# Kernel tuning notes

Hardware: AMD Instinct MI355X
Metric: run time of the kernel (lower is better)

Reference implementation:

```python
import jax, jax.numpy as jnp
import numpy as np

B_, K_, D_, L_, N_, R_ = 2, 4, 128, 4096, 16, 8


def setup_inputs() -> dict:
    key = jax.random.key(0)
    ks = jax.random.split(key, 7)
    return {
        "q_x": jax.random.normal(ks[0], (B_, K_, D_, L_), jnp.float32),
        "kv_x": jax.random.normal(ks[1], (B_, K_, D_, L_), jnp.float32),
        "x_proj_weight": jax.random.normal(ks[2], (K_, R_ + 2 * N_, D_), jnp.float32) * 0.02,
        "dt_projs_weight": jax.random.normal(ks[3], (K_, D_, R_), jnp.float32) * 0.02,
        "dt_projs_bias": jax.random.normal(ks[4], (K_, D_), jnp.float32) * 0.1,
        "A_logs": jax.random.uniform(ks[5], (K_ * D_, N_), jnp.float32),
        "Ds": jax.random.normal(ks[6], (K_ * D_,), jnp.float32),
    }


def _selective_scan(u, delta, A, Bmat, Cmat, Ds):
    # u, delta: [B,K,D,L]; A: [K,D,N]; Bmat, Cmat: [B,K,N,L]; Ds: [K,D]
    uT = jnp.moveaxis(u, -1, 0)      # [L,B,K,D]
    dT = jnp.moveaxis(delta, -1, 0)  # [L,B,K,D]
    BT = jnp.moveaxis(Bmat, -1, 0)   # [L,B,K,N]
    CT = jnpp if False else jnp.moveaxis(Cmat, -1, 0)  # [L,B,K,N]
    h0 = jnp.zeros(u.shape[:3] + (A.shape[-1],), jnp.float32)  # [B,K,D,N]

    def step(h, xs):
        u_l, d_l, B_l, C_l = xs
        dA = jnp.exp(d_l[..., None] * A)  # [B,K,D,N]
        h = dA * h + (d_l * u_l)[..., None] * B_l[:, :, None, :]
        y = jnp.einsum('bkdn,bkn->bkd', h, C_l)
        return h, y

    _, yT = jax.lax.scan(step, h0, (uT, dT, BT, CT))
    y = jnp.moveaxis(yT, 0, -1)  # [B,K,D,L]
    return y + u * Ds[None, :, :, None]


def reference(q_x, kv_x, x_proj_weight, dt_projs_weight, dt_projs_bias, A_logs, Ds):
    B, K, D, L = kv_x.shape
    N = A_logs.shape[1]
    R = dt_projs_weight.shape[2]
    # projections of kv (for dt, B) and q (for C)
    x_dbl = jnp.einsum('bkdl,kcd->bkcl', kv_x, x_proj_weight)
    x_c = jnp.einsum('bkdl,kcd->bkcl', q_x, x_proj_weight)
    dts = x_dbl[:, :, :R]          # [B,K,R,L]
    Bs = x_dbl[:, :, R:R + N]      # [B,K,N,L]
    Cs = x_c[:, :, R + N:]         # [B,K,N,L]
    dts = jnp.einsum('bkrl,kdr->bkdl', dts, dt_projs_weight)
    A = -jnp.exp(A_logs.astype(jnp.float32)).reshape(K, D, N)
    delta = jax.nn.softplus(dts.astype(jnp.float32) + dt_projs_bias.astype(jnp.float32)[None, :, :, None])
    y = _selective_scan(kv_x.astype(jnp.float32), delta, A,
                        Bs.astype(jnp.float32), Cs.astype(jnp.float32),
                        Ds.astype(jnp.float32).reshape(K, D))
    return y  # [B,K,D,L] float32
```

## Files before the change

### kernel.cpp

```cpp
#include <hip/hip_runtime.h>
#include <cmath>

namespace {
constexpr int B_ = 2, K_ = 4, D_ = 128, L_ = 4096, N_ = 16, R_ = 8, C_ = 40;
constexpr int CHUNK = 32, NCH = L_ / CHUNK;
constexpr float LOG2E = 1.44269504f;
}

#if __has_builtin(__builtin_amdgcn_exp2f)
#define FEXP2(x) __builtin_amdgcn_exp2f(x)
#else
#define FEXP2(x) exp2f(x)
#endif

__global__ __launch_bounds__(640, 2) void k1_proj(
    const float* __restrict__ qx, const float* __restrict__ kv,
    const float* __restrict__ xw,
    float* __restrict__ dtsT,
    float* __restrict__ BT,
    float* __restrict__ CT)
{
    __shared__ float Wt[D_ * C_];

    const int tid = threadIdx.x;
    const int w = tid >> 6, lane = tid & 63;
    const int dg = lane >> 5, lq = lane & 31;
    int blk = blockIdx.x;
    const int lt = blk & 31; blk >>= 5;
    const int k = blk & 3; const int b = blk >> 2;
    const int bk = b * K_ + k;

    for (int i = tid; i < C_ * D_; i += 640) {
        const int c = i >> 7, d = i & 127;
        Wt[d * C_ + c] = xw[(k * C_ + c) * D_ + d];
    }
    __syncthreads();

    const float* xsrc = (w >= 6) ? qx : kv;
    const int c0 = w * 4;
    float acc[4][4];
    #pragma unroll
    for (int c = 0; c < 4; ++c)
        #pragma unroll
        for (int j = 0; j < 4; ++j) acc[c][j] = 0.f;

    const float* src = xsrc + ((size_t)bk * D_ + dg * 64) * L_ + lt * 128 + 4 * lq;
    #pragma unroll 8
    for (int dd = 0; dd < 64; ++dd) {
        const float4 x = *(const float4*)(src + (size_t)dd * L_);
        const float4 wv = *(const float4*)&Wt[(dg * 64 + dd) * C_ + c0];
        const float* wp = (const float*)&wv;
        #pragma unroll
        for (int c = 0; c < 4; ++c) {
            acc[c][0] = fmaf(x.x, wp[c], acc[c][0]);
            acc[c][1] = fmaf(x.y, wp[c], acc[c][1]);
            acc[c][2] = fmaf(x.z, wp[c], acc[c][2]);
            acc[c][3] = fmaf(x.w, wp[c], acc[c][3]);
        }
    }

    #pragma unroll
    for (int c = 0; c < 4; ++c)
        #pragma unroll
        for (int j = 0; j < 4; ++j)
            acc[c][j] += __shfl_xor(acc[c][j], 32, 64);

    if (dg == 0) {
        #pragma unroll
        for (int j = 0; j < 4; ++j) {
            const int l = lt * 128 + 4 * lq + j;
            float4 o; o.x = acc[0][j]; o.y = acc[1][j]; o.z = acc[2][j]; o.w = acc[3][j];
            if (w < 2)
                *(float4*)(dtsT + ((size_t)bk * L_ + l) * R_ + w * 4) = o;
            else if (w < 6)
                *(float4*)(BT + ((size_t)bk * L_ + l) * N_ + (w - 2) * 4) = o;
            else
                *(float4*)(CT + ((size_t)bk * L_ + l) * N_ + (w - 6) * 4) = o;
        }
    }
}

__global__ __launch_bounds__(128, 1) void k2_pass1(
    const float* __restrict__ kv, const float* __restrict__ dtsT,
    const float* __restrict__ BT, const float* __restrict__ alg,
    const float* __restrict__ dtw, const float* __restrict__ dtb,
    float* __restrict__ hend, float* __restrict__ Ssum)
{
    __shared__ float dts_s[CHUNK * R_];
    __shared__ float B_s[CHUNK * N_];

    const int tid = threadIdx.x;
    const int d = tid;
    const int blk = blockIdx.x;
    const int ch = blk & (NCH - 1);
    const int bk = blk >> 7;
    const int k = bk & 3;

    {
        const float* src = dtsT + ((size_t)bk * L_ + ch * CHUNK) * R_;
        if (tid < 64) *(float4*)&dts_s[4 * tid] = *(const float4*)(src + 4 * tid);
        const float* bsrc = BT + ((size_t)bk * L_ + ch * CHUNK) * N_;
        *(float4*)&B_s[4 * tid] = *(const float4*)(bsrc + 4 * tid);
    }

    float uu[CHUNK];
    {
        const float4* up = (const float4*)(kv + ((size_t)bk * D_ + d) * L_ + ch * CHUNK);
        #pragma unroll
        for (int j = 0; j < 8; ++j) {
            const float4 v = up[j];
            uu[4*j] = v.x; uu[4*j+1] = v.y; uu[4*j+2] = v.z; uu[4*j+3] = v.w;
        }
    }

    float dtwr[R_];
    {
        const float* p = dtw + ((size_t)k * D_ + d) * R_;
        *(float4*)&dtwr[0] = *(const float4*)p;
        *(float4*)&dtwr[4] = *(const float4*)(p + 4);
    }
    const float bias = dtb[k * D_ + d];
    float A2[N_];
    {
        const float* ap = alg + ((size_t)k * D_ + d) * N_;
        #pragma unroll
        for (int j = 0; j < 4; ++j) {
            float4 a = *(const float4*)(ap + 4 * j);
            A2[4*j]   = -__expf(a.x) * LOG2E; A2[4*j+1] = -__expf(a.y) * LOG2E;
            A2[4*j+2] = -__expf(a.z) * LOG2E; A2[4*j+3] = -__expf(a.w) * LOG2E;
        }
    }
    __syncthreads();

    float h[N_];
    #pragma unroll
    for (int n = 0; n < N_; ++n) h[n] = 0.f;
    float sd = 0.f;

    #pragma unroll
    for (int l = 0; l < CHUNK; ++l) {
        float dv[R_];
        *(float4*)&dv[0] = *(const float4*)&dts_s[l * R_];
        *(float4*)&dv[4] = *(const float4*)&dts_s[l * R_ + 4];
        float s = bias;
        #pragma unroll
        for (int r = 0; r < R_; ++r) s = fmaf(dv[r], dtwr[r], s);
        const float e = FEXP2(s * LOG2E);
        const float dlt = (s > 15.f) ? s : __logf(1.f + e);
        sd += dlt;
        const float xb = dlt * uu[l];
        #pragma unroll
        for (int g = 0; g < 4; ++g) {
            const float4 bg = *(const float4*)&B_s[l * N_ + 4 * g];
            h[4*g+0] = fmaf(FEXP2(dlt * A2[4*g+0]), h[4*g+0], xb * bg.x);
            h[4*g+1] = fmaf(FEXP2(dlt * A2[4*g+1]), h[4*g+1], xb * bg.y);
            h[4*g+2] = fmaf(FEXP2(dlt * A2[4*g+2]), h[4*g+2], xb * bg.z);
            h[4*g+3] = fmaf(FEXP2(dlt * A2[4*g+3]), h[4*g+3], xb * bg.w);
        }
    }

    float* hp = hend + (((size_t)bk * NCH + ch) * D_ + d) * N_;
    #pragma unroll
    for (int j = 0; j < 4; ++j) {
        float4 o; o.x = h[4*j]; o.y = h[4*j+1]; o.z = h[4*j+2]; o.w = h[4*j+3];
        *(float4*)(hp + 4 * j) = o;
    }
    Ssum[((size_t)bk * NCH + ch) * D_ + d] = sd;
}

__global__ __launch_bounds__(64, 2) void k25_chain(
    const float* __restrict__ alg, const float* __restrict__ Ssum,
    const float* __restrict__ hend, float* __restrict__ hinit)
{
    const int tg = blockIdx.x * 64 + threadIdx.x;
    const int n = tg & 15;
    const int d = (tg >> 4) & 127;
    const int bk = tg >> 11;
    const int k = bk & 3;

    const float A2 = -__expf(alg[((size_t)k * D_ + d) * N_ + n]) * LOG2E;
    float h = 0.f;
    for (int c0 = 0; c0 < NCH; c0 += 32) {
        float he[32], ss[32];
        #pragma unroll
        for (int j = 0; j < 32; ++j) {
            const size_t si = ((size_t)bk * NCH + c0 + j) * D_ + d;
            he[j] = hend[si * N_ + n];
            ss[j] = Ssum[si];
        }
        #pragma unroll
        for (int j = 0; j < 32; ++j) {
            const size_t si = ((size_t)bk * NCH + c0 + j) * D_ + d;
            hinit[si * N_ + n] = h;
            h = fmaf(FEXP2(ss[j] * A2), h, he[j]);
        }
    }
}

__global__ __launch_bounds__(128, 1) void k3_pass2(
    const float* __restrict__ kv, const float* __restrict__ dtsT,
    const float* __restrict__ BT, const float* __restrict__ CT,
    const float* __restrict__ alg, const float* __restrict__ dtw,
    const float* __restrict__ dtb, const float* __restrict__ DsG,
    const float* __restrict__ hinit, float* __restrict__ out)
{
    constexpr int YS = CHUNK + 1;
    __shared__ float dts_s[CHUNK * R_];
    __shared__ float B_s[CHUNK * N_];
    __shared__ float C_s[CHUNK * N_];
    __shared__ float y_s[D_ * YS];

    const int tid = threadIdx.x;
    const int d = tid;
    const int blk = blockIdx.x;
    const int ch = blk & (NCH - 1);
    const int bk = blk >> 7;
    const int k = bk & 3;

    {
        const float* src = dtsT + ((size_t)bk * L_ + ch * CHUNK) * R_;
        if (tid < 64) *(float4*)&dts_s[4 * tid] = *(const float4*)(src + 4 * tid);
        const float* bsrc = BT + ((size_t)bk * L_ + ch * CHUNK) * N_;
        *(float4*)&B_s[4 * tid] = *(const float4*)(bsrc + 4 * tid);
        const float* csrc = CT + ((size_t)bk * L_ + ch * CHUNK) * N_;
        *(float4*)&C_s[4 * tid] = *(const float4*)(csrc + 4 * tid);
    }

    float uu[CHUNK];
    {
        const float4* up = (const float4*)(kv + ((size_t)bk * D_ + d) * L_ + ch * CHUNK);
        #pragma unroll
        for (int j = 0; j < 8; ++j) {
            const float4 v = up[j];
            uu[4*j] = v.x; uu[4*j+1] = v.y; uu[4*j+2] = v.z; uu[4*j+3] = v.w;
        }
    }

    float dtwr[R_];
    {
        const float* p = dtw + ((size_t)k * D_ + d) * R_;
        *(float4*)&dtwr[0] = *(const float4*)p;
        *(float4*)&dtwr[4] = *(const float4*)(p + 4);
    }
    const float bias = dtb[k * D_ + d];
    const float Dv = DsG[k * D_ + d];
    float A2[N_];
    {
        const float* ap = alg + ((size_t)k * D_ + d) * N_;
        #pragma unroll
        for (int j = 0; j < 4; ++j) {
            float4 a = *(const float4*)(ap + 4 * j);
            A2[4*j]   = -__expf(a.x) * LOG2E; A2[4*j+1] = -__expf(a.y) * LOG2E;
            A2[4*j+2] = -__expf(a.z) * LOG2E; A2[4*j+3] = -__expf(a.w) * LOG2E;
        }
    }

    float h[N_];
    {
        const float* hp = hinit + (((size_t)bk * NCH + ch) * D_ + d) * N_;
        #pragma unroll
        for (int j = 0; j < 4; ++j) {
            float4 v = *(const float4*)(hp + 4 * j);
            h[4*j] = v.x; h[4*j+1] = v.y; h[4*j+2] = v.z; h[4*j+3] = v.w;
        }
    }
    __syncthreads();

    #pragma unroll
    for (int l = 0; l < CHUNK; ++l) {
        float dv[R_];
        *(float4*)&dv[0] = *(const float4*)&dts_s[l * R_];
        *(float4*)&dv[4] = *(const float4*)&dts_s[l * R_ + 4];
        float s = bias;
        #pragma unroll
        for (int r = 0; r < R_; ++r) s = fmaf(dv[r], dtwr[r], s);
        const float e = FEXP2(s * LOG2E);
        const float dlt = (s > 15.f) ? s : __logf(1.f + e);
        const float xb = dlt * uu[l];
        float p0 = 0.f, p1 = 0.f;
        #pragma unroll
        for (int g = 0; g < 4; ++g) {
            const float4 bg = *(const float4*)&B_s[l * N_ + 4 * g];
            const float4 cg = *(const float4*)&C_s[l * N_ + 4 * g];
            h[4*g+0] = fmaf(FEXP2(dlt * A2[4*g+0]), h[4*g+0], xb * bg.x);
            p0 = fmaf(h[4*g+0], cg.x, p0);
            h[4*g+1] = fmaf(FEXP2(dlt * A2[4*g+1]), h[4*g+1], xb * bg.y);
            p1 = fmaf(h[4*g+1], cg.y, p1);
            h[4*g+2] = fmaf(FEXP2(dlt * A2[4*g+2]), h[4*g+2], xb * bg.z);
            p0 = fmaf(h[4*g+2], cg.z, p0);
            h[4*g+3] = fmaf(FEXP2(dlt * A2[4*g+3]), h[4*g+3], xb * bg.w);
            p1 = fmaf(h[4*g+3], cg.w, p1);
        }
        y_s[d * YS + l] = fmaf(uu[l], Dv, p0 + p1);
    }
    __syncthreads();

    #pragma unroll
    for (int p = 0; p < 8; ++p) {
        const int f = tid + p * 128;
        const int row = f >> 3, j4 = (f & 7) * 4;
        const float* yp = &y_s[row * YS + j4];
        float4 o; o.x = yp[0]; o.y = yp[1]; o.z = yp[2]; o.w = yp[3];
        *(float4*)(out + ((size_t)bk * D_ + row) * L_ + ch * CHUNK + j4) = o;
    }
}

extern "C" void kernel_launch(void* const* d_in, const int* in_sizes, int n_in,
                              void* d_out, int out_size, void* d_ws, size_t ws_size,
                              hipStream_t stream)
{
    const float* qx  = (const float*)d_in[0];
    const float* kv  = (const float*)d_in[1];
    const float* xw  = (const float*)d_in[2];
    const float* dtw = (const float*)d_in[3];
    const float* dtb = (const float*)d_in[4];
    const float* alg = (const float*)d_in[5];
    const float* Ds  = (const float*)d_in[6];
    float* out = (float*)d_out;

    const size_t sz_dts = (size_t)B_ * K_ * L_ * R_;
    const size_t sz_bc  = (size_t)B_ * K_ * L_ * N_;
    const size_t sz_h   = (size_t)B_ * K_ * NCH * D_ * N_;
    const size_t sz_ss  = (size_t)B_ * K_ * NCH * D_;
    const size_t need = (sz_dts + 2 * sz_bc + 2 * sz_h + sz_ss) * sizeof(float);
    if (ws_size < need) return;

    float* dts   = (float*)d_ws;
    float* BTp   = dts + sz_dts;
    float* CTp   = BTp + sz_bc;
    float* hend  = CTp + sz_bc;
    float* hinit = hend + sz_h;
    float* Ssm   = hinit + sz_h;

    k1_proj<<<B_ * K_ * 32, 640, 0, stream>>>(qx, kv, xw, dts, BTp, CTp);
    k2_pass1<<<B_ * K_ * NCH, 128, 0, stream>>>(kv, dts, BTp, alg, dtw, dtb, hend, Ssm);
    k25_chain<<<256, 64, 0, stream>>>(alg, Ssm, hend, hinit);
    k3_pass2<<<B_ * K_ * NCH, 128, 0, stream>>>(kv, dts, BTp, CTp, alg, dtw, dtb, Ds, hinit, out);
}
```

Baseline: 63.74 us.

## Fuse projection and scan pass-1 kernels into one launch

Merges the x-projection kernel and the first chunked-scan pass into one kernel of 512 threads per block. Each block computes the dt, B and C projections for 128 positions and writes them to the workspace. After a block barrier it reloads dt and B into shared memory and runs the pass-1 scan over four 32-long chunks. This removes one kernel launch and the inter-kernel gap. In exchange, the projection now has 8 waves for 10 jobs, so two waves do double work. It also relies on global writes being visible within the block after __syncthreads.

```diff
diff --git a/kernel.cpp b/kernel.cpp
--- a/kernel.cpp
+++ b/kernel.cpp
@@ -13,95 +13,86 @@
 #define FEXP2(x) exp2f(x)
 #endif
 
-__global__ __launch_bounds__(640, 2) void k1_proj(
+__global__ __launch_bounds__(512) void kA_proj_pass1(
     const float* __restrict__ qx, const float* __restrict__ kv,
-    const float* __restrict__ xw,
-    float* __restrict__ dtsT,
-    float* __restrict__ BT,
-    float* __restrict__ CT)
+    const float* __restrict__ xw, const float* __restrict__ dtw,
+    const float* __restrict__ dtb, const float* __restrict__ alg,
+    float* __restrict__ dtsT, float* __restrict__ BT, float* __restrict__ CT,
+    float* __restrict__ hend, float* __restrict__ Ssum)
 {
     __shared__ float Wt[D_ * C_];
+    __shared__ float dts_s[128 * R_];
+    __shared__ float B_s[128 * N_];
 
     const int tid = threadIdx.x;
     const int w = tid >> 6, lane = tid & 63;
-    const int dg = lane >> 5, lq = lane & 31;
-    int blk = blockIdx.x;
-    const int lt = blk & 31; blk >>= 5;
-    const int k = blk & 3; const int b = blk >> 2;
-    const int bk = b * K_ + k;
-
-    for (int i = tid; i < C_ * D_; i += 640) {
-        const int c = i >> 7, d = i & 127;
-        Wt[d * C_ + c] = xw[(k * C_ + c) * D_ + d];
-    }
-    __syncthreads();
-
-    const float* xsrc = (w >= 6) ? qx : kv;
-    const int c0 = w * 4;
-    float acc[4][4];
-    #pragma unroll
-    for (int c = 0; c < 4; ++c)
-        #pragma unroll
-        for (int j = 0; j < 4; ++j) acc[c][j] = 0.f;
-
-    const float* src = xsrc + ((size_t)bk * D_ + dg * 64) * L_ + lt * 128 + 4 * lq;
-    #pragma unroll 8
-    for (int dd = 0; dd < 64; ++dd) {
-        const float4 x = *(const float4*)(src + (size_t)dd * L_);
-        const float4 wv = *(const float4*)&Wt[(dg * 64 + dd) * C_ + c0];
-        const float* wp = (const float*)&wv;
-        #pragma unroll
-        for (int c = 0; c < 4; ++c) {
-            acc[c][0] = fmaf(x.x, wp[c], acc[c][0]);
-            acc[c][1] = fmaf(x.y, wp[c], acc[c][1]);
-            acc[c][2] = fmaf(x.z, wp[c], acc[c][2]);
-            acc[c][3] = fmaf(x.w, wp[c], acc[c][3]);
-        }
-    }
-
-    #pragma unroll
-    for (int c = 0; c < 4; ++c)
-        #pragma unroll
-        for (int j = 0; j < 4; ++j)
-            acc[c][j] += __shfl_xor(acc[c][j], 32, 64);
-
-    if (dg == 0) {
-        #pragma unroll
-        for (int j = 0; j < 4; ++j) {
-            const int l = lt * 128 + 4 * lq + j;
-            float4 o; o.x = acc[0][j]; o.y = acc[1][j]; o.z = acc[2][j]; o.w = acc[3][j];
-            if (w < 2)
-                *(float4*)(dtsT + ((size_t)bk * L_ + l) * R_ + w * 4) = o;
-            else if (w < 6)
-                *(float4*)(BT + ((size_t)bk * L_ + l) * N_ + (w - 2) * 4) = o;
-            else
-                *(float4*)(CT + ((size_t)bk * L_ + l) * N_ + (w - 6) * 4) = o;
-        }
-    }
-}
-
-__global__ __launch_bounds__(128, 1) void k2_pass1(
-    const float* __restrict__ kv, const float* __restrict__ dtsT,
-    const float* __restrict__ BT, const float* __restrict__ alg,
-    const float* __restrict__ dtw, const float* __restrict__ dtb,
-    float* __restrict__ hend, float* __restrict__ Ssum)
-{
-    __shared__ float dts_s[CHUNK * R_];
-    __shared__ float B_s[CHUNK * N_];
-
-    const int tid = threadIdx.x;
-    const int d = tid;
-    const int blk = blockIdx.x;
-    const int ch = blk & (NCH - 1);
-    const int bk = blk >> 7;
-    const int k = bk & 3;
-
-    {
-        const float* src = dtsT + ((size_t)bk * L_ + ch * CHUNK) * R_;
-        if (tid < 64) *(float4*)&dts_s[4 * tid] = *(const float4*)(src + 4 * tid);
-        const float* bsrc = BT + ((size_t)bk * L_ + ch * CHUNK) * N_;
-        *(float4*)&B_s[4 * tid] = *(const float4*)(bsrc + 4 * tid);
-    }
+    const int bk = blockIdx.x >> 5;
+    const int k  = bk & 3;
+    const int lt = blockIdx.x & 31;
+
+    for (int i = tid; i < C_ * D_; i += 512) {
+        const int c = i >> 7, dd = i & 127;
+        Wt[dd * C_ + c] = xw[(k * C_ + c) * D_ + dd];
+    }
+    __syncthreads();
+    {
+        const int dg = lane >> 5, lq = lane & 31;
+        for (int job = w; job < 10; job += 8) {
+            const float* xsrc = (job >= 6) ? qx : kv;
+            const int c0 = job * 4;
+            float acc[4][4];
+            #pragma unroll
+            for (int c = 0; c < 4; ++c)
+                #pragma unroll
+                for (int j = 0; j < 4; ++j) acc[c][j] = 0.f;
+
+            const float* src = xsrc + ((size_t)bk * D_ + dg * 64) * L_ + lt * 128 + 4 * lq;
+            #pragma unroll 8
+            for (int dd = 0; dd < 64; ++dd) {
+                const float4 x = *(const float4*)(src + (size_t)dd * L_);
+                const float4 wv = *(const float4*)&Wt[(dg * 64 + dd) * C_ + c0];
+                const float* wp = (const float*)&wv;
+                #pragma unroll
+                for (int c = 0; c < 4; ++c) {
+                    acc[c][0] = fmaf(x.x, wp[c], acc[c][0]);
+                    acc[c][1] = fmaf(x.y, wp[c], acc[c][1]);
+                    acc[c][2] = fmaf(x.z, wp[c], acc[c][2]);
+                    acc[c][3] = fmaf(x.w, wp[c], acc[c][3]);
+                }
+            }
+            #pragma unroll
+            for (int c = 0; c < 4; ++c)
+                #pragma unroll
+                for (int j = 0; j < 4; ++j)
+                    acc[c][j] += __shfl_xor(acc[c][j], 32, 64);
+
+            if (dg == 0) {
+                #pragma unroll
+                for (int j = 0; j < 4; ++j) {
+                    const int l = lt * 128 + 4 * lq + j;
+                    float4 o; o.x = acc[0][j]; o.y = acc[1][j]; o.z = acc[2][j]; o.w = acc[3][j];
+                    if (job < 2)
+                        *(float4*)(dtsT + ((size_t)bk * L_ + l) * R_ + job * 4) = o;
+                    else if (job < 6)
+                        *(float4*)(BT + ((size_t)bk * L_ + l) * N_ + (job - 2) * 4) = o;
+                    else
+                        *(float4*)(CT + ((size_t)bk * L_ + l) * N_ + (job - 6) * 4) = o;
+                }
+            }
+        }
+    }
+    __syncthreads();
+
+    {
+        const float4* s1 = (const float4*)(dtsT + ((size_t)bk * L_ + lt * 128) * R_);
+        if (tid < 256) ((float4*)dts_s)[tid] = s1[tid];
+        const float4* s2 = (const float4*)(BT + ((size_t)bk * L_ + lt * 128) * N_);
+        ((float4*)B_s)[tid] = s2[tid];
+    }
+
+    const int chl = tid >> 7;
+    const int d   = tid & 127;
+    const int ch  = lt * 4 + chl;
 
     float uu[CHUNK];
     {
@@ -112,7 +103,6 @@
             uu[4*j] = v.x; uu[4*j+1] = v.y; uu[4*j+2] = v.z; uu[4*j+3] = v.w;
         }
     }
-
     float dtwr[R_];
     {
         const float* p = dtw + ((size_t)k * D_ + d) * R_;
@@ -139,26 +129,26 @@
 
     #pragma unroll
     for (int l = 0; l < CHUNK; ++l) {
+        const int ll = chl * 32 + l;
         float dv[R_];
-        *(float4*)&dv[0] = *(const float4*)&dts_s[l * R_];
-        *(float4*)&dv[4] = *(const float4*)&dts_s[l * R_ + 4];
+        *(float4*)&dv[0] = *(const float4*)&dts_s[ll * R_];
+        *(float4*)&dv[4] = *(const float4*)&dts_s[ll * R_ + 4];
         float s = bias;
         #pragma unroll
         for (int r = 0; r < R_; ++r) s = fmaf(dv[r], dtwr[r], s);
         const float e = FEXP2(s * LOG2E);
-        const float dlt = (s > 15.f) ? s : __logf(1.f + e);
-        sd += dlt;
-        const float xb = dlt * uu[l];
+        const float dl = (s > 15.f) ? s : __logf(1.f + e);
+        sd += dl;
+        const float xb = dl * uu[l];
         #pragma unroll
         for (int g = 0; g < 4; ++g) {
-            const float4 bg = *(const float4*)&B_s[l * N_ + 4 * g];
-            h[4*g+0] = fmaf(FEXP2(dlt * A2[4*g+0]), h[4*g+0], xb * bg.x);
-            h[4*g+1] = fmaf(FEXP2(dlt * A2[4*g+1]), h[4*g+1], xb * bg.y);
-            h[4*g+2] = fmaf(FEXP2(dlt * A2[4*g+2]), h[4*g+2], xb * bg.z);
-            h[4*g+3] = fmaf(FEXP2(dlt * A2[4*g+3]), h[4*g+3], xb * bg.w);
-        }
-    }
-
+            const float4 bg = *(const float4*)&B_s[ll * N_ + 4 * g];
+            h[4*g+0] = fmaf(FEXP2(dl * A2[4*g+0]), h[4*g+0], xb * bg.x);
+            h[4*g+1] = fmaf(FEXP2(dl * A2[4*g+1]), h[4*g+1], xb * bg.y);
+            h[4*g+2] = fmaf(FEXP2(dl * A2[4*g+2]), h[4*g+2], xb * bg.z);
+            h[4*g+3] = fmaf(FEXP2(dl * A2[4*g+3]), h[4*g+3], xb * bg.w);
+        }
+    }
     float* hp = hend + (((size_t)bk * NCH + ch) * D_ + d) * N_;
     #pragma unroll
     for (int j = 0; j < 4; ++j) {
@@ -209,7 +199,6 @@
     __shared__ float B_s[CHUNK * N_];
     __shared__ float C_s[CHUNK * N_];
     __shared__ float y_s[D_ * YS];
-
     const int tid = threadIdx.x;
     const int d = tid;
     const int blk = blockIdx.x;
@@ -225,7 +214,6 @@
         const float* csrc = CT + ((size_t)bk * L_ + ch * CHUNK) * N_;
         *(float4*)&C_s[4 * tid] = *(const float4*)(csrc + 4 * tid);
     }
-
     float uu[CHUNK];
     {
         const float4* up = (const float4*)(kv + ((size_t)bk * D_ + d) * L_ + ch * CHUNK);
@@ -235,7 +223,6 @@
             uu[4*j] = v.x; uu[4*j+1] = v.y; uu[4*j+2] = v.z; uu[4*j+3] = v.w;
         }
     }
-
     float dtwr[R_];
     {
         const float* p = dtw + ((size_t)k * D_ + d) * R_;
@@ -254,7 +241,6 @@
             A2[4*j+2] = -__expf(a.z) * LOG2E; A2[4*j+3] = -__expf(a.w) * LOG2E;
         }
     }
-
     float h[N_];
     {
         const float* hp = hinit + (((size_t)bk * NCH + ch) * D_ + d) * N_;
@@ -281,15 +267,15 @@
         #pragma unroll
         for (int g = 0; g < 4; ++g) {
             const float4 bg = *(const float4*)&B_s[l * N_ + 4 * g];
-            const float4 cg = *(const float4*)&C_s[l * N_ + 4 * g];
+            const float4 cg4 = *(const float4*)&C_s[l * N_ + 4 * g];
             h[4*g+0] = fmaf(FEXP2(dlt * A2[4*g+0]), h[4*g+0], xb * bg.x);
-            p0 = fmaf(h[4*g+0], cg.x, p0);
+            p0 = fmaf(h[4*g+0], cg4.x, p0);
             h[4*g+1] = fmaf(FEXP2(dlt * A2[4*g+1]), h[4*g+1], xb * bg.y);
-            p1 = fmaf(h[4*g+1], cg.y, p1);
+            p1 = fmaf(h[4*g+1], cg4.y, p1);
             h[4*g+2] = fmaf(FEXP2(dlt * A2[4*g+2]), h[4*g+2], xb * bg.z);
-            p0 = fmaf(h[4*g+2], cg.z, p0);
+            p0 = fmaf(h[4*g+2], cg4.z, p0);
             h[4*g+3] = fmaf(FEXP2(dlt * A2[4*g+3]), h[4*g+3], xb * bg.w);
-            p1 = fmaf(h[4*g+3], cg.w, p1);
+            p1 = fmaf(h[4*g+3], cg4.w, p1);
         }
         y_s[d * YS + l] = fmaf(uu[l], Dv, p0 + p1);
     }
@@ -332,8 +318,8 @@
     float* hinit = hend + sz_h;
     float* Ssm   = hinit + sz_h;
 
-    k1_proj<<<B_ * K_ * 32, 640, 0, stream>>>(qx, kv, xw, dts, BTp, CTp);
-    k2_pass1<<<B_ * K_ * NCH, 128, 0, stream>>>(kv, dts, BTp, alg, dtw, dtb, hend, Ssm);
+    kA_proj_pass1<<<B_ * K_ * 32, 512, 0, stream>>>(qx, kv, xw, dtw, dtb, alg,
+                                                    dts, BTp, CTp, hend, Ssm);
     k25_chain<<<256, 64, 0, stream>>>(alg, Ssm, hend, hinit);
     k3_pass2<<<B_ * K_ * NCH, 128, 0, stream>>>(kv, dts, BTp, CTp, alg, dtw, dtb, Ds, hinit, out);
 }
```

New measurement: 72.63 us. 1.14x slower.

## Restructure projection kernel to stage X tile in LDS and split kv/q blocks

Applied to the files above, without the earlier changes.

The projection kernel is rewritten so each block loads a 128x128 tile of either kv_x or q_x into shared memory and computes only the channels that input needs: 24 channels (dt and B) from kv, 16 channels (C) from q. Before, each of the ten waves read its own slice of X from global memory, so kv was read repeatedly for every channel group. The grid doubles to 512 blocks of 192 threads, which reduces redundant global traffic and the cross-half shuffle reduction. In exchange, each block uses about 76 KB of LDS, which limits occupancy, and in q blocks two of the six waves do nothing.

```diff
diff --git a/kernel.cpp b/kernel.cpp
--- a/kernel.cpp
+++ b/kernel.cpp
@@ -13,69 +13,74 @@
 #define FEXP2(x) exp2f(x)
 #endif
 
-__global__ __launch_bounds__(640, 2) void k1_proj(
+__global__ __launch_bounds__(192, 2) void kP_gemm(
     const float* __restrict__ qx, const float* __restrict__ kv,
     const float* __restrict__ xw,
     float* __restrict__ dtsT,
     float* __restrict__ BT,
     float* __restrict__ CT)
 {
-    __shared__ float Wt[D_ * C_];
+    __shared__ float Xs[128 * 128];
+    __shared__ float Ws[128 * 24];
 
     const int tid = threadIdx.x;
-    const int w = tid >> 6, lane = tid & 63;
-    const int dg = lane >> 5, lq = lane & 31;
-    int blk = blockIdx.x;
-    const int lt = blk & 31; blk >>= 5;
-    const int k = blk & 3; const int b = blk >> 2;
-    const int bk = b * K_ + k;
-
-    for (int i = tid; i < C_ * D_; i += 640) {
-        const int c = i >> 7, d = i & 127;
-        Wt[d * C_ + c] = xw[(k * C_ + c) * D_ + d];
+    const int typ = blockIdx.x & 1;
+    const int lt  = (blockIdx.x >> 1) & 31;
+    const int bk  = blockIdx.x >> 6;
+    const int k   = bk & 3;
+    const float* X = typ ? qx : kv;
+
+    if (typ == 0) {
+        for (int i = tid; i < 24 * D_; i += 192) {
+            const int c = i % 24, d = i / 24;
+            Ws[d * 24 + c] = xw[(k * C_ + c) * D_ + d];
+        }
+    } else {
+        for (int i = tid; i < 16 * D_; i += 192) {
+            const int c = i & 15, d = i >> 4;
+            Ws[d * 16 + c] = xw[(k * C_ + 24 + c) * D_ + d];
+        }
+    }
+    {
+        const float* src = X + (size_t)bk * D_ * L_ + lt * 128;
+        for (int f = tid; f < 4096; f += 192) {
+            const int d = f >> 5, l4 = (f & 31) << 2;
+            *(float4*)&Xs[d * 128 + l4] = *(const float4*)(src + (size_t)d * L_ + l4);
+        }
     }
     __syncthreads();
 
-    const float* xsrc = (w >= 6) ? qx : kv;
-    const int c0 = w * 4;
-    float acc[4][4];
-    #pragma unroll
-    for (int c = 0; c < 4; ++c)
-        #pragma unroll
-        for (int j = 0; j < 4; ++j) acc[c][j] = 0.f;
-
-    const float* src = xsrc + ((size_t)bk * D_ + dg * 64) * L_ + lt * 128 + 4 * lq;
-    #pragma unroll 8
-    for (int dd = 0; dd < 64; ++dd) {
-        const float4 x = *(const float4*)(src + (size_t)dd * L_);
-        const float4 wv = *(const float4*)&Wt[(dg * 64 + dd) * C_ + c0];
-        const float* wp = (const float*)&wv;
-        #pragma unroll
-        for (int c = 0; c < 4; ++c) {
-            acc[c][0] = fmaf(x.x, wp[c], acc[c][0]);
-            acc[c][1] = fmaf(x.y, wp[c], acc[c][1]);
-            acc[c][2] = fmaf(x.z, wp[c], acc[c][2]);
-            acc[c][3] = fmaf(x.w, wp[c], acc[c][3]);
-        }
-    }
-
-    #pragma unroll
-    for (int c = 0; c < 4; ++c)
-        #pragma unroll
-        for (int j = 0; j < 4; ++j)
-            acc[c][j] += __shfl_xor(acc[c][j], 32, 64);
-
-    if (dg == 0) {
+    const int cg = tid >> 5;
+    const int lp = tid & 31;
+    const int NC = typ ? 16 : 24;
+    if (cg * 4 < NC) {
+        const int ch = cg * 4;
+        float acc[4][4];
+        #pragma unroll
+        for (int c = 0; c < 4; ++c)
+            #pragma unroll
+            for (int j = 0; j < 4; ++j) acc[c][j] = 0.f;
+
+        #pragma unroll 4
+        for (int d = 0; d < D_; ++d) {
+            const float4 xv = *(const float4*)&Xs[d * 128 + lp * 4];
+            const float4 wv = *(const float4*)&Ws[d * NC + ch];
+            const float* xp = (const float*)&xv;
+            const float* wp = (const float*)&wv;
+            #pragma unroll
+            for (int c = 0; c < 4; ++c)
+                #pragma unroll
+                for (int j = 0; j < 4; ++j)
+                    acc[c][j] = fmaf(xp[j], wp[c], acc[c][j]);
+        }
+
+        const size_t base = (size_t)bk * L_ + lt * 128 + lp * 4;
         #pragma unroll
         for (int j = 0; j < 4; ++j) {
-            const int l = lt * 128 + 4 * lq + j;
             float4 o; o.x = acc[0][j]; o.y = acc[1][j]; o.z = acc[2][j]; o.w = acc[3][j];
-            if (w < 2)
-                *(float4*)(dtsT + ((size_t)bk * L_ + l) * R_ + w * 4) = o;
-            else if (w < 6)
-                *(float4*)(BT + ((size_t)bk * L_ + l) * N_ + (w - 2) * 4) = o;
-            else
-                *(float4*)(CT + ((size_t)bk * L_ + l) * N_ + (w - 6) * 4) = o;
+            if (typ)          *(float4*)(CT + (base + j) * N_ + ch) = o;
+            else if (ch < 8)  *(float4*)(dtsT + (base + j) * R_ + ch) = o;
+            else              *(float4*)(BT + (base + j) * N_ + (ch - 8)) = o;
         }
     }
 }
@@ -209,7 +214,6 @@
     __shared__ float B_s[CHUNK * N_];
     __shared__ float C_s[CHUNK * N_];
     __shared__ float y_s[D_ * YS];
-
     const int tid = threadIdx.x;
     const int d = tid;
     const int blk = blockIdx.x;
@@ -225,7 +229,6 @@
         const float* csrc = CT + ((size_t)bk * L_ + ch * CHUNK) * N_;
         *(float4*)&C_s[4 * tid] = *(const float4*)(csrc + 4 * tid);
     }
-
     float uu[CHUNK];
     {
         const float4* up = (const float4*)(kv + ((size_t)bk * D_ + d) * L_ + ch * CHUNK);
@@ -235,7 +238,6 @@
             uu[4*j] = v.x; uu[4*j+1] = v.y; uu[4*j+2] = v.z; uu[4*j+3] = v.w;
         }
     }
-
     float dtwr[R_];
     {
         const float* p = dtw + ((size_t)k * D_ + d) * R_;
@@ -254,7 +256,6 @@
             A2[4*j+2] = -__expf(a.z) * LOG2E; A2[4*j+3] = -__expf(a.w) * LOG2E;
         }
     }
-
     float h[N_];
     {
         const float* hp = hinit + (((size_t)bk * NCH + ch) * D_ + d) * N_;
@@ -281,15 +282,15 @@
         #pragma unroll
         for (int g = 0; g < 4; ++g) {
             const float4 bg = *(const float4*)&B_s[l * N_ + 4 * g];
-            const float4 cg = *(const float4*)&C_s[l * N_ + 4 * g];
+            const float4 cg4 = *(const float4*)&C_s[l * N_ + 4 * g];
             h[4*g+0] = fmaf(FEXP2(dlt * A2[4*g+0]), h[4*g+0], xb * bg.x);
-            p0 = fmaf(h[4*g+0], cg.x, p0);
+            p0 = fmaf(h[4*g+0], cg4.x, p0);
             h[4*g+1] = fmaf(FEXP2(dlt * A2[4*g+1]), h[4*g+1], xb * bg.y);
-            p1 = fmaf(h[4*g+1], cg.y, p1);
+            p1 = fmaf(h[4*g+1], cg4.y, p1);
             h[4*g+2] = fmaf(FEXP2(dlt * A2[4*g+2]), h[4*g+2], xb * bg.z);
-            p0 = fmaf(h[4*g+2], cg.z, p0);
+            p0 = fmaf(h[4*g+2], cg4.z, p0);
             h[4*g+3] = fmaf(FEXP2(dlt * A2[4*g+3]), h[4*g+3], xb * bg.w);
-            p1 = fmaf(h[4*g+3], cg.w, p1);
+            p1 = fmaf(h[4*g+3], cg4.w, p1);
         }
         y_s[d * YS + l] = fmaf(uu[l], Dv, p0 + p1);
     }
@@ -332,7 +333,7 @@
     float* hinit = hend + sz_h;
     float* Ssm   = hinit + sz_h;
 
-    k1_proj<<<B_ * K_ * 32, 640, 0, stream>>>(qx, kv, xw, dts, BTp, CTp);
+    kP_gemm<<<B_ * K_ * 32 * 2, 192, 0, stream>>>(qx, kv, xw, dts, BTp, CTp);
     k2_pass1<<<B_ * K_ * NCH, 128, 0, stream>>>(kv, dts, BTp, alg, dtw, dtb, hend, Ssm);
     k25_chain<<<256, 64, 0, stream>>>(alg, Ssm, hend, hinit);
     k3_pass2<<<B_ * K_ * NCH, 128, 0, stream>>>(kv, dts, BTp, CTp, alg, dtw, dtb, Ds, hinit, out);
```

New measurement: 76.52 us. 1.2x slower.

## Make chunked scan hierarchical: group chunks in pass1, shorten the serial chain

Applied to the files above, without the earlier changes.

Pass 1 now processes groups of 4 chunks per block. It records each chunk's prefix state and prefix delta-sum inside the group, plus the group-end state. The serial chain kernel then runs over 32 groups instead of 128 chunks. Pass 2 rebuilds each chunk's initial state from the group initial state and the stored prefix. This shortens the latency-bound sequential chain, at the cost of 4x fewer pass-1 blocks (256 instead of 1024) and extra prefix-state writes and reads.

```diff
diff --git a/kernel.cpp b/kernel.cpp
--- a/kernel.cpp
+++ b/kernel.cpp
@@ -4,6 +4,8 @@
 namespace {
 constexpr int B_ = 2, K_ = 4, D_ = 128, L_ = 4096, N_ = 16, R_ = 8, C_ = 40;
 constexpr int CHUNK = 32, NCH = L_ / CHUNK;
+constexpr int GC = 4, GL = GC * CHUNK;
+constexpr int NG = NCH / GC;
 constexpr float LOG2E = 1.44269504f;
 }
 
@@ -16,9 +18,7 @@
 __global__ __launch_bounds__(640, 2) void k1_proj(
     const float* __restrict__ qx, const float* __restrict__ kv,
     const float* __restrict__ xw,
-    float* __restrict__ dtsT,
-    float* __restrict__ BT,
-    float* __restrict__ CT)
+    float* __restrict__ dtsT, float* __restrict__ BT, float* __restrict__ CT)
 {
     __shared__ float Wt[D_ * C_];
 
@@ -80,15 +80,155 @@
     }
 }
 
-__global__ __launch_bounds__(128, 1) void k2_pass1(
+__global__ __launch_bounds__(128, 1) void k2v2_pass1(
     const float* __restrict__ kv, const float* __restrict__ dtsT,
     const float* __restrict__ BT, const float* __restrict__ alg,
     const float* __restrict__ dtw, const float* __restrict__ dtb,
-    float* __restrict__ hend, float* __restrict__ Ssum)
-{
+    float* __restrict__ hpart,
+    float* __restrict__ Spre,
+    float* __restrict__ hgend,
+    float* __restrict__ Sgrp)
+{
+    __shared__ float dts_s[GL * R_];
+    __shared__ float B_s[GL * N_];
+
+    const int tid = threadIdx.x;
+    const int d = tid;
+    const int g  = blockIdx.x & (NG - 1);
+    const int bk = blockIdx.x >> 5;
+    const int k = bk & 3;
+    const int l0 = g * GL;
+
+    {
+        const float4* src = (const float4*)(dtsT + ((size_t)bk * L_ + l0) * R_);
+        ((float4*)dts_s)[tid]       = src[tid];
+        ((float4*)dts_s)[tid + 128] = src[tid + 128];
+        const float4* bsrc = (const float4*)(BT + ((size_t)bk * L_ + l0) * N_);
+        #pragma unroll
+        for (int f = 0; f < 4; ++f)
+            ((float4*)B_s)[tid + f * 128] = bsrc[tid + f * 128];
+    }
+
+    float dtwr[R_];
+    {
+        const float* p = dtw + ((size_t)k * D_ + d) * R_;
+        *(float4*)&dtwr[0] = *(const float4*)p;
+        *(float4*)&dtwr[4] = *(const float4*)(p + 4);
+    }
+    const float bias = dtb[k * D_ + d];
+    float A2[N_];
+    {
+        const float* ap = alg + ((size_t)k * D_ + d) * N_;
+        #pragma unroll
+        for (int j = 0; j < 4; ++j) {
+            float4 a = *(const float4*)(ap + 4 * j);
+            A2[4*j]   = -__expf(a.x) * LOG2E; A2[4*j+1] = -__expf(a.y) * LOG2E;
+            A2[4*j+2] = -__expf(a.z) * LOG2E; A2[4*j+3] = -__expf(a.w) * LOG2E;
+        }
+    }
+    __syncthreads();
+
+    float h[N_];
+    #pragma unroll
+    for (int n = 0; n < N_; ++n) h[n] = 0.f;
+    float sd = 0.f;
+
+    #pragma unroll
+    for (int p = 0; p < GC; ++p) {
+        const int ch = g * GC + p;
+        {
+            float* hp = hpart + (((size_t)bk * NCH + ch) * D_ + d) * N_;
+            #pragma unroll
+            for (int j = 0; j < 4; ++j) {
+                float4 o; o.x = h[4*j]; o.y = h[4*j+1]; o.z = h[4*j+2]; o.w = h[4*j+3];
+                *(float4*)(hp + 4 * j) = o;
+            }
+            Spre[((size_t)bk * NCH + ch) * D_ + d] = sd;
+        }
+        float uu[CHUNK];
+        {
+            const float4* up = (const float4*)(kv + ((size_t)bk * D_ + d) * L_ + ch * CHUNK);
+            #pragma unroll
+            for (int j = 0; j < 8; ++j) {
+                const float4 v = up[j];
+                uu[4*j] = v.x; uu[4*j+1] = v.y; uu[4*j+2] = v.z; uu[4*j+3] = v.w;
+            }
+        }
+        #pragma unroll
+        for (int l = 0; l < CHUNK; ++l) {
+            const int ll = p * CHUNK + l;
+            float dv[R_];
+            *(float4*)&dv[0] = *(const float4*)&dts_s[ll * R_];
+            *(float4*)&dv[4] = *(const float4*)&dts_s[ll * R_ + 4];
+            float s = bias;
+            #pragma unroll
+            for (int r = 0; r < R_; ++r) s = fmaf(dv[r], dtwr[r], s);
+            const float e = FEXP2(s * LOG2E);
+            const float dlt = (s > 15.f) ? s : __logf(1.f + e);
+            sd += dlt;
+            const float xb = dlt * uu[l];
+            #pragma unroll
+            for (int gg = 0; gg < 4; ++gg) {
+                const float4 bg = *(const float4*)&B_s[ll * N_ + 4 * gg];
+                h[4*gg+0] = fmaf(FEXP2(dlt * A2[4*gg+0]), h[4*gg+0], xb * bg.x);
+                h[4*gg+1] = fmaf(FEXP2(dlt * A2[4*gg+1]), h[4*gg+1], xb * bg.y);
+                h[4*gg+2] = fmaf(FEXP2(dlt * A2[4*gg+2]), h[4*gg+2], xb * bg.z);
+                h[4*gg+3] = fmaf(FEXP2(dlt * A2[4*gg+3]), h[4*gg+3], xb * bg.w);
+            }
+        }
+    }
+
+    {
+        float* hp = hgend + (((size_t)bk * NG + g) * D_ + d) * N_;
+        #pragma unroll
+        for (int j = 0; j < 4; ++j) {
+            float4 o; o.x = h[4*j]; o.y = h[4*j+1]; o.z = h[4*j+2]; o.w = h[4*j+3];
+            *(float4*)(hp + 4 * j) = o;
+        }
+        Sgrp[((size_t)bk * NG + g) * D_ + d] = sd;
+    }
+}
+
+__global__ __launch_bounds__(64, 2) void k25b_chain(
+    const float* __restrict__ alg, const float* __restrict__ Sgrp,
+    const float* __restrict__ hgend, float* __restrict__ hginit)
+{
+    const int tg = blockIdx.x * 64 + threadIdx.x;
+    const int n = tg & 15;
+    const int d = (tg >> 4) & 127;
+    const int bk = tg >> 11;
+    const int k = bk & 3;
+
+    const float A2 = -__expf(alg[((size_t)k * D_ + d) * N_ + n]) * LOG2E;
+    float he[NG], ss[NG];
+    #pragma unroll
+    for (int j = 0; j < NG; ++j) {
+        const size_t si = ((size_t)bk * NG + j) * D_ + d;
+        he[j] = hgend[si * N_ + n];
+        ss[j] = Sgrp[si];
+    }
+    float h = 0.f;
+    #pragma unroll
+    for (int j = 0; j < NG; ++j) {
+        const size_t si = ((size_t)bk * NG + j) * D_ + d;
+        hginit[si * N_ + n] = h;
+        h = fmaf(FEXP2(ss[j] * A2), h, he[j]);
+    }
+}
+
+__global__ __launch_bounds__(128, 1) void k3_pass2(
+    const float* __restrict__ kv, const float* __restrict__ dtsT,
+    const float* __restrict__ BT, const float* __restrict__ CT,
+    const float* __restrict__ alg, const float* __restrict__ dtw,
+    const float* __restrict__ dtb, const float* __restrict__ DsG,
+    const float* __restrict__ hpart, const float* __restrict__ Spre,
+    const float* __restrict__ hginit, float* __restrict__ out)
+{
+    constexpr int YS = CHUNK + 1;
     __shared__ float dts_s[CHUNK * R_];
     __shared__ float B_s[CHUNK * N_];
-
+    __shared__ float C_s[CHUNK * N_];
+    __shared__ float y_s[D_ * YS];
     const int tid = threadIdx.x;
     const int d = tid;
     const int blk = blockIdx.x;
@@ -101,8 +241,9 @@
         if (tid < 64) *(float4*)&dts_s[4 * tid] = *(const float4*)(src + 4 * tid);
         const float* bsrc = BT + ((size_t)bk * L_ + ch * CHUNK) * N_;
         *(float4*)&B_s[4 * tid] = *(const float4*)(bsrc + 4 * tid);
-    }
-
+        const float* csrc = CT + ((size_t)bk * L_ + ch * CHUNK) * N_;
+        *(float4*)&C_s[4 * tid] = *(const float4*)(csrc + 4 * tid);
+    }
     float uu[CHUNK];
     {
         const float4* up = (const float4*)(kv + ((size_t)bk * D_ + d) * L_ + ch * CHUNK);
@@ -112,7 +253,6 @@
             uu[4*j] = v.x; uu[4*j+1] = v.y; uu[4*j+2] = v.z; uu[4*j+3] = v.w;
         }
     }
-
     float dtwr[R_];
     {
         const float* p = dtw + ((size_t)k * D_ + d) * R_;
@@ -120,6 +260,7 @@
         *(float4*)&dtwr[4] = *(const float4*)(p + 4);
     }
     const float bias = dtb[k * D_ + d];
+    const float Dv = DsG[k * D_ + d];
     float A2[N_];
     {
         const float* ap = alg + ((size_t)k * D_ + d) * N_;
@@ -130,12 +271,22 @@
             A2[4*j+2] = -__expf(a.z) * LOG2E; A2[4*j+3] = -__expf(a.w) * LOG2E;
         }
     }
+    float h[N_];
+    {
+        const float Sp = Spre[((size_t)bk * NCH + ch) * D_ + d];
+        const float* hp = hpart + (((size_t)bk * NCH + ch) * D_ + d) * N_;
+        const float* hg = hginit + (((size_t)bk * NG + (ch >> 2)) * D_ + d) * N_;
+        #pragma unroll
+        for (int j = 0; j < 4; ++j) {
+            float4 vp = *(const float4*)(hp + 4 * j);
+            float4 vg = *(const float4*)(hg + 4 * j);
+            h[4*j+0] = fmaf(FEXP2(Sp * A2[4*j+0]), vg.x, vp.x);
+            h[4*j+1] = fmaf(FEXP2(Sp * A2[4*j+1]), vg.y, vp.y);
+            h[4*j+2] = fmaf(FEXP2(Sp * A2[4*j+2]), vg.z, vp.z);
+            h[4*j+3] = fmaf(FEXP2(Sp * A2[4*j+3]), vg.w, vp.w);
+        }
+    }
     __syncthreads();
-
-    float h[N_];
-    #pragma unroll
-    for (int n = 0; n < N_; ++n) h[n] = 0.f;
-    float sd = 0.f;
 
     #pragma unroll
     for (int l = 0; l < CHUNK; ++l) {
@@ -147,149 +298,20 @@
         for (int r = 0; r < R_; ++r) s = fmaf(dv[r], dtwr[r], s);
         const float e = FEXP2(s * LOG2E);
         const float dlt = (s > 15.f) ? s : __logf(1.f + e);
-        sd += dlt;
         const float xb = dlt * uu[l];
+        float p0 = 0.f, p1 = 0.f;
         #pragma unroll
         for (int g = 0; g < 4; ++g) {
             const float4 bg = *(const float4*)&B_s[l * N_ + 4 * g];
+            const float4 cg4 = *(const float4*)&C_s[l * N_ + 4 * g];
             h[4*g+0] = fmaf(FEXP2(dlt * A2[4*g+0]), h[4*g+0], xb * bg.x);
+            p0 = fmaf(h[4*g+0], cg4.x, p0);
             h[4*g+1] = fmaf(FEXP2(dlt * A2[4*g+1]), h[4*g+1], xb * bg.y);
+            p1 = fmaf(h[4*g+1], cg4.y, p1);
             h[4*g+2] = fmaf(FEXP2(dlt * A2[4*g+2]), h[4*g+2], xb * bg.z);
+            p0 = fmaf(h[4*g+2], cg4.z, p0);
             h[4*g+3] = fmaf(FEXP2(dlt * A2[4*g+3]), h[4*g+3], xb * bg.w);
-        }
-    }
-
-    float* hp = hend + (((size_t)bk * NCH + ch) * D_ + d) * N_;
-    #pragma unroll
-    for (int j = 0; j < 4; ++j) {
-        float4 o; o.x = h[4*j]; o.y = h[4*j+1]; o.z = h[4*j+2]; o.w = h[4*j+3];
-        *(float4*)(hp + 4 * j) = o;
-    }
-    Ssum[((size_t)bk * NCH + ch) * D_ + d] = sd;
-}
-
-__global__ __launch_bounds__(64, 2) void k25_chain(
-    const float* __restrict__ alg, const float* __restrict__ Ssum,
-    const float* __restrict__ hend, float* __restrict__ hinit)
-{
-    const int tg = blockIdx.x * 64 + threadIdx.x;
-    const int n = tg & 15;
-    const int d = (tg >> 4) & 127;
-    const int bk = tg >> 11;
-    const int k = bk & 3;
-
-    const float A2 = -__expf(alg[((size_t)k * D_ + d) * N_ + n]) * LOG2E;
-    float h = 0.f;
-    for (int c0 = 0; c0 < NCH; c0 += 32) {
-        float he[32], ss[32];
-        #pragma unroll
-        for (int j = 0; j < 32; ++j) {
-            const size_t si = ((size_t)bk * NCH + c0 + j) * D_ + d;
-            he[j] = hend[si * N_ + n];
-            ss[j] = Ssum[si];
-        }
-        #pragma unroll
-        for (int j = 0; j < 32; ++j) {
-            const size_t si = ((size_t)bk * NCH + c0 + j) * D_ + d;
-            hinit[si * N_ + n] = h;
-            h = fmaf(FEXP2(ss[j] * A2), h, he[j]);
-        }
-    }
-}
-
-__global__ __launch_bounds__(128, 1) void k3_pass2(
-    const float* __restrict__ kv, const float* __restrict__ dtsT,
-    const float* __restrict__ BT, const float* __restrict__ CT,
-    const float* __restrict__ alg, const float* __restrict__ dtw,
-    const float* __restrict__ dtb, const float* __restrict__ DsG,
-    const float* __restrict__ hinit, float* __restrict__ out)
-{
-    constexpr int YS = CHUNK + 1;
-    __shared__ float dts_s[CHUNK * R_];
-    __shared__ float B_s[CHUNK * N_];
-    __shared__ float C_s[CHUNK * N_];
-    __shared__ float y_s[D_ * YS];
-
-    const int tid = threadIdx.x;
-    const int d = tid;
-    const int blk = blockIdx.x;
-    const int ch = blk & (NCH - 1);
-    const int bk = blk >> 7;
-    const int k = bk & 3;
-
-    {
-        const float* src = dtsT + ((size_t)bk * L_ + ch * CHUNK) * R_;
-        if (tid < 64) *(float4*)&dts_s[4 * tid] = *(const float4*)(src + 4 * tid);
-        const float* bsrc = BT + ((size_t)bk * L_ + ch * CHUNK) * N_;
-        *(float4*)&B_s[4 * tid] = *(const float4*)(bsrc + 4 * tid);
-        const float* csrc = CT + ((size_t)bk * L_ + ch * CHUNK) * N_;
-        *(float4*)&C_s[4 * tid] = *(const float4*)(csrc + 4 * tid);
-    }
-
-    float uu[CHUNK];
-    {
-        const float4* up = (const float4*)(kv + ((size_t)bk * D_ + d) * L_ + ch * CHUNK);
-        #pragma unroll
-        for (int j = 0; j < 8; ++j) {
-            const float4 v = up[j];
-            uu[4*j] = v.x; uu[4*j+1] = v.y; uu[4*j+2] = v.z; uu[4*j+3] = v.w;
-        }
-    }
-
-    float dtwr[R_];
-    {
-        const float* p = dtw + ((size_t)k * D_ + d) * R_;
-        *(float4*)&dtwr[0] = *(const float4*)p;
-        *(float4*)&dtwr[4] = *(const float4*)(p + 4);
-    }
-    const float bias = dtb[k * D_ + d];
-    const float Dv = DsG[k * D_ + d];
-    float A2[N_];
-    {
-        const float* ap = alg + ((size_t)k * D_ + d) * N_;
-        #pragma unroll
-        for (int j = 0; j < 4; ++j) {
-            float4 a = *(const float4*)(ap + 4 * j);
-            A2[4*j]   = -__expf(a.x) * LOG2E; A2[4*j+1] = -__expf(a.y) * LOG2E;
-            A2[4*j+2] = -__expf(a.z) * LOG2E; A2[4*j+3] = -__expf(a.w) * LOG2E;
-        }
-    }
-
-    float h[N_];
-    {
-        const float* hp = hinit + (((size_t)bk * NCH + ch) * D_ + d) * N_;
-        #pragma unroll
-        for (int j = 0; j < 4; ++j) {
-            float4 v = *(const float4*)(hp + 4 * j);
-            h[4*j] = v.x; h[4*j+1] = v.y; h[4*j+2] = v.z; h[4*j+3] = v.w;
-        }
-    }
-    __syncthreads();
-
-    #pragma unroll
-    for (int l = 0; l < CHUNK; ++l) {
-        float dv[R_];
-        *(float4*)&dv[0] = *(const float4*)&dts_s[l * R_];
-        *(float4*)&dv[4] = *(const float4*)&dts_s[l * R_ + 4];
-        float s = bias;
-        #pragma unroll
-        for (int r = 0; r < R_; ++r) s = fmaf(dv[r], dtwr[r], s);
-        const float e = FEXP2(s * LOG2E);
-        const float dlt = (s > 15.f) ? s : __logf(1.f + e);
-        const float xb = dlt * uu[l];
-        float p0 = 0.f, p1 = 0.f;
-        #pragma unroll
-        for (int g = 0; g < 4; ++g) {
-            const float4 bg = *(const float4*)&B_s[l * N_ + 4 * g];
-            const float4 cg = *(const float4*)&C_s[l * N_ + 4 * g];
-            h[4*g+0] = fmaf(FEXP2(dlt * A2[4*g+0]), h[4*g+0], xb * bg.x);
-            p0 = fmaf(h[4*g+0], cg.x, p0);
-            h[4*g+1] = fmaf(FEXP2(dlt * A2[4*g+1]), h[4*g+1], xb * bg.y);
-            p1 = fmaf(h[4*g+1], cg.y, p1);
-            h[4*g+2] = fmaf(FEXP2(dlt * A2[4*g+2]), h[4*g+2], xb * bg.z);
-            p0 = fmaf(h[4*g+2], cg.z, p0);
-            h[4*g+3] = fmaf(FEXP2(dlt * A2[4*g+3]), h[4*g+3], xb * bg.w);
-            p1 = fmaf(h[4*g+3], cg.w, p1);
+            p1 = fmaf(h[4*g+3], cg4.w, p1);
         }
         y_s[d * YS + l] = fmaf(uu[l], Dv, p0 + p1);
     }
@@ -318,22 +340,28 @@
     const float* Ds  = (const float*)d_in[6];
     float* out = (float*)d_out;
 
-    const size_t sz_dts = (size_t)B_ * K_ * L_ * R_;
-    const size_t sz_bc  = (size_t)B_ * K_ * L_ * N_;
-    const size_t sz_h   = (size_t)B_ * K_ * NCH * D_ * N_;
-    const size_t sz_ss  = (size_t)B_ * K_ * NCH * D_;
-    const size_t need = (sz_dts + 2 * sz_bc + 2 * sz_h + sz_ss) * sizeof(float);
+    const size_t sz_dts  = (size_t)B_ * K_ * L_ * R_;
+    const size_t sz_bc   = (size_t)B_ * K_ * L_ * N_;
+    const size_t sz_hp   = (size_t)B_ * K_ * NCH * D_ * N_;
+    const size_t sz_sp   = (size_t)B_ * K_ * NCH * D_;
+    const size_t sz_hg   = (size_t)B_ * K_ * NG * D_ * N_;
+    const size_t sz_sg   = (size_t)B_ * K_ * NG * D_;
+    const size_t need = (sz_dts + 2 * sz_bc + sz_hp + sz_sp + 2 * sz_hg + sz_sg) * sizeof(float);
     if (ws_size < need) return;
 
-    float* dts   = (float*)d_ws;
-    float* BTp   = dts + sz_dts;
-    float* CTp   = BTp + sz_bc;
-    float* hend  = CTp + sz_bc;
-    float* hinit = hend + sz_h;
-    float* Ssm   = hinit + sz_h;
+    float* dts    = (float*)d_ws;
+    float* BTp    = dts + sz_dts;
+    float* CTp    = BTp + sz_bc;
+    float* hpart  = CTp + sz_bc;
+    float* Spre   = hpart + sz_hp;
+    float* hgend  = Spre + sz_sp;
+    float* hginit = hgend + sz_hg;
+    float* Sgrp   = hginit + sz_hg;
 
     k1_proj<<<B_ * K_ * 32, 640, 0, stream>>>(qx, kv, xw, dts, BTp, CTp);
-    k2_pass1<<<B_ * K_ * NCH, 128, 0, stream>>>(kv, dts, BTp, alg, dtw, dtb, hend, Ssm);
-    k25_chain<<<256, 64, 0, stream>>>(alg, Ssm, hend, hinit);
-    k3_pass2<<<B_ * K_ * NCH, 128, 0, stream>>>(kv, dts, BTp, CTp, alg, dtw, dtb, Ds, hinit, out);
-}
+    k2v2_pass1<<<B_ * K_ * NG, 128, 0, stream>>>(kv, dts, BTp, alg, dtw, dtb,
+                                                 hpart, Spre, hgend, Sgrp);
+    k25b_chain<<<256, 64, 0, stream>>>(alg, Sgrp, hgend, hginit);
+    k3_pass2<<<B_ * K_ * NCH, 128, 0, stream>>>(kv, dts, BTp, CTp, alg, dtw, dtb,
+                                                Ds, hpart, Spre, hginit, out);
+}
```

Measured after the change: 78.03 us. 22.4% more time.
